# Performance work log

Hardware: AMD Instinct MI355X
Metric: run time of the kernel (lower is better)

Reference implementation:

```python
import jax, jax.numpy as jnp
import numpy as np

B, T, DIN, DM, NC = 8, 4096, 1024, 256, 157
DILS = (1, 2, 4, 8, 16)


def _conv1(w, x, b=None):
    # 1x1 conv: w [out,in], x [B,in,T] -> [B,out,T]
    y = jnp.einsum('oi,bit->bot', w, x)
    return y if b is None else y + b[None, :, None]


def _dal(x, wq, wk, wv, d):
    # Dilated 3-tap multiplicative local attention (DAL block, groups=1).
    # Taps in the zero-padded (pad=d) sequence at offsets 0, d, 2d == positions t-d, t, t+d.
    _, _, T_ = x.shape
    xp = jnp.pad(x, ((0, 0), (0, 0), (d, d)))
    q = _conv1(wq, x)                 # [B,C,T]
    kp = _conv1(wk, xp)               # [B,C,T+2d]
    vp = _conv1(wv, xp)
    k = jnp.stack([kp[:, :, 0:T_], kp[:, :, d:T_ + d], kp[:, :, 2 * d:T_ + 2 * d]], axis=-1)  # [B,C,T,3]
    v = jnp.stack([vp[:, :, 0:T_], vp[:, :, d:T_ + d], vp[:, :, 2 * d:T_ + 2 * d]], axis=-1)
    attn = jax.nn.softmax(q[..., None] * k, axis=-1)  # softmax over the 3 taps
    return jnp.sum(attn * v, axis=-1)  # [B,C,T]


def _fwd(x, mask, bottle0_w, bottle0_b,
         dal1_wq, dal1_wk, dal1_wv, bottle1_w, bottle1_b,
         dal2_wq, dal2_wk, dal2_wv, bottle2_w, bottle2_b,
         dal3_wq, dal3_wk, dal3_wv, bottle3_w, bottle3_b,
         dal4_wq, dal4_wk, dal4_wv, bottle4_w, bottle4_b,
         dal5_wq, dal5_wk, dal5_wv, bottle5_w, bottle5_b,
         bottle6_w, bottle6_b):
    m = mask[:, 0:1, :]
    out = _conv1(bottle0_w, x, bottle0_b)
    layers = [
        (dal1_wq, dal1_wk, dal1_wv, bottle1_w, bottle1_b),
        (dal2_wq, dal2_wk, dal2_wv, bottle2_w, bottle2_b),
        (dal3_wq, dal3_wk, dal3_wv, bottle3_w, bottle3_b),
        (dal4_wq, dal4_wk, dal4_wv, bottle4_w, bottle4_b),
        (dal5_wq, dal5_wk, dal5_wv, bottle5_w, bottle5_b),
    ]
    # Dropout layers are identity in eval mode.
    for (wq, wk, wv, bw, bb), d in zip(layers, DILS):
        h = jax.nn.relu(_dal(out, wq, wk, wv, d))
        h = _conv1(bw, h, bb)
        out = (out + h) * m
    return _conv1(bottle6_w, out, bottle6_b) * m  # [B,NC,T]


def setup_inputs() -> dict:
    key = jax.random.key(0)
    ks = jax.random.split(key, 32)
    s = 0.05
    inp = {}
    inp['x'] = jax.random.normal(ks[0], (B, DIN, T), jnp.float32)
    inp['mask'] = jnp.ones((B, 1, T), jnp.float32)
    inp['bottle0_w'] = jax.random.normal(ks[1], (DM, DIN), jnp.float32) * s
    inp['bottle0_b'] = jnp.zeros((DM,), jnp.float32)
    i = 2
    for l in range(1, 6):
        inp['dal%d_wq' % l] = jax.random.normal(ks[i], (DM, DM), jnp.float32) * s; i += 1
        inp['dal%d_wk' % l] = jax.random.normal(ks[i], (DM, DM), jnp.float32) * s; i += 1
        inp['dal%d_wv' % l] = jax.random.normal(ks[i], (DM, DM), jnp.float32) * s; i += 1
        inp['bottle%d_w' % l] = jax.random.normal(ks[i], (DM, DM), jnp.float32) * s; i += 1
        inp['bottle%d_b' % l] = jnp.zeros((DM,), jnp.float32)
    inp['bottle6_w'] = jax.random.normal(ks[i], (NC, DM), jnp.float32) * s
    inp['bottle6_b'] = jnp.zeros((NC,), jnp.float32)
    return inp


def reference(x, mask, bottle0_w, bottle0_b,
              dal1_wq, dal1_wk, dal1_wv, bottle1_w, bottle1_b,
              dal2_wq, dal2_wk, dal2_wv, bottle2_w, bottle2_b,
              dal3_wq, dal3_wk, dal3_wv, bottle3_w, bottle3_b,
              dal4_wq, dal4_wk, dal4_wv, bottle4_w, bottle4_b,
              dal5_wq, dal5_wk, dal5_wv, bottle5_w, bottle5_b,
              bottle6_w, bottle6_b):
    return _fwd(x, mask, bottle0_w, bottle0_b,
                dal1_wq, dal1_wk, dal1_wv, bottle1_w, bottle1_b,
                dal2_wq, dal2_wk, dal2_wv, bottle2_w, bottle2_b,
                dal3_wq, dal3_wk, dal3_wv, bottle3_w, bottle3_b,
                dal4_wq, dal4_wk, dal4_wv, bottle4_w, bottle4_b,
                dal5_wq, dal5_wk, dal5_wv, bottle5_w, bottle5_b,
                bottle6_w, bottle6_b)
```

## Files before the change

### kernel.cpp

```cpp
#include <hip/hip_runtime.h>
#include <hip/hip_bf16.h>
#include <stdint.h>

#define T_LEN 4096
#define B_SZ  8
#define D_IN  1024
#define D_M   256
#define N_C   157

typedef __attribute__((ext_vector_type(8))) short short8;
typedef __attribute__((ext_vector_type(4))) float floatx4;

static __device__ __forceinline__ unsigned short f2bf(float f) {
  unsigned u = __float_as_uint(f);
  u += 0x7FFFu + ((u >> 16) & 1u);
  return (unsigned short)(u >> 16);
}
static __device__ __forceinline__ float bf2f(unsigned short h) {
  return __uint_as_float(((unsigned)h) << 16);
}

static __device__ __forceinline__ void gl_lds16(const unsigned short* g,
                                                unsigned short* l) {
  __builtin_amdgcn_global_load_lds(
      (const __attribute__((address_space(1))) unsigned int*)g,
      (__attribute__((address_space(3))) unsigned int*)l, 16, 0, 0);
}

struct WSeg { const float* src; int n; int off; };
struct WPrepArgs { WSeg seg[22]; };

__global__ void wprep_kernel(WPrepArgs a, unsigned short* __restrict__ wbuf) {
  WSeg s = a.seg[blockIdx.x];
  for (int i = (blockIdx.y << 8) + threadIdx.x; i < s.n; i += (gridDim.y << 8))
    wbuf[s.off + i] = f2bf(s.src[i]);
}

__global__ void transpose_xT(const float* __restrict__ x,
                             unsigned short* __restrict__ xT) {
  __shared__ float tile[64][65];
  const int t0 = blockIdx.x << 6;
  const int i0 = blockIdx.y << 6;
  const int b  = blockIdx.z;
  const int tid = threadIdx.x;
  {
    const int row = tid >> 2;
    const int cc  = (tid & 3) << 4;
    const float* src = x + ((size_t)b * D_IN + (i0 + row)) * T_LEN + t0 + cc;
#pragma unroll
    for (int p = 0; p < 4; ++p) {
      float4 v = *(const float4*)(src + p * 4);
      tile[row][cc + p * 4 + 0] = v.x;
      tile[row][cc + p * 4 + 1] = v.y;
      tile[row][cc + p * 4 + 2] = v.z;
      tile[row][cc + p * 4 + 3] = v.w;
    }
  }
  __syncthreads();
#pragma unroll
  for (int it = 0; it < 2; ++it) {
    const int task = tid + (it << 8);
    const int tr = task >> 3;
    const int ic = (task & 7) << 3;
    short8 o;
#pragma unroll
    for (int j = 0; j < 8; ++j) o[j] = (short)f2bf(tile[ic + j][tr]);
    *(short8*)(xT + ((size_t)b * T_LEN + (t0 + tr)) * D_IN + i0 + ic) = o;
  }
}

template<bool ATTN, bool HAS_BIAS, bool HAS_RES, bool HAS_MASK,
         bool WRITE_BF16, bool OUT_CT_F32>
__global__ __launch_bounds__(256)
void gemm_kernel(const unsigned short* __restrict__ Xact,
                 const unsigned short* __restrict__ W,
                 const float* __restrict__ bias,
                 const unsigned short* __restrict__ residB,
                 const float* __restrict__ mask,
                 float* __restrict__ outF,
                 unsigned short* __restrict__ outB,
                 int K, int Mw, int dil) {
  __shared__ unsigned short sA[128 * 64];
  __shared__ unsigned short sB[128 * 64];

  const int n0 = blockIdx.x << 7;
  const int t0 = blockIdx.y << 7;
  const int b  = blockIdx.z;
  const int tid = threadIdx.x;
  const int wv   = tid >> 6;
  const int lane = tid & 63;
  const int wm = (wv >> 1) << 6;
  const int wn = (wv & 1) << 6;
  const int fm = lane & 15;
  const int fq = lane >> 4;
  const int lrow = lane >> 3;
  const int cbg8 = (((lane & 7) ^ lrow) << 3);

  const unsigned short* Xb =
      Xact + (size_t)b * T_LEN * (size_t)(ATTN ? 768 : K);

  const short8 z8 = {0, 0, 0, 0, 0, 0, 0, 0};
  const floatx4 fz = {0.f, 0.f, 0.f, 0.f};
  floatx4 acc[4][4];
#pragma unroll
  for (int i = 0; i < 4; ++i)
#pragma unroll
    for (int j = 0; j < 4; ++j) acc[i][j] = fz;

  for (int kk = 0; kk < K; kk += 64) {
    if constexpr (ATTN) {
#pragma unroll
      for (int it = 0; it < 4; ++it) {
        int c = tid + (it << 8);
        int m = c >> 3;
        int cb = c & 7;
        int ch = kk + (cb << 3);
        int t = t0 + m;
        const unsigned short* base = Xb + (size_t)t * 768 + ch;
        short8 qv = *(const short8*)(base);
        short8 kc = *(const short8*)(base + 256);
        short8 vc = *(const short8*)(base + 512);
        short8 km = z8, kp = z8, vm = z8, vp = z8;
        const long off = (long)dil * 768;
        if (t >= dil) {
          km = *(const short8*)(base - off + 256);
          vm = *(const short8*)(base - off + 512);
        }
        if (t + dil < T_LEN) {
          kp = *(const short8*)(base + off + 256);
          vp = *(const short8*)(base + off + 512);
        }
        short8 o;
#pragma unroll
        for (int e = 0; e < 8; ++e) {
          float q  = bf2f((unsigned short)qv[e]);
          float s0 = q * bf2f((unsigned short)km[e]);
          float s1 = q * bf2f((unsigned short)kc[e]);
          float s2 = q * bf2f((unsigned short)kp[e]);
          float mx = fmaxf(s0, fmaxf(s1, s2));
          float e0 = __expf(s0 - mx), e1 = __expf(s1 - mx), e2 = __expf(s2 - mx);
          float num = e0 * bf2f((unsigned short)vm[e]) +
                      e1 * bf2f((unsigned short)vc[e]) +
                      e2 * bf2f((unsigned short)vp[e]);
          float r = num / (e0 + e1 + e2);
          o[e] = (short)f2bf(fmaxf(r, 0.0f));
        }
        *(short8*)&sA[(m << 6) + ((cb ^ (m & 7)) << 3)] = o;
      }
    } else {
#pragma unroll
      for (int p = 0; p < 4; ++p) {
        const int slot = (p << 2) + wv;
        gl_lds16(Xb + (size_t)(t0 + (slot << 3) + lrow) * K + kk + cbg8,
                 sA + slot * 512);
      }
    }
#pragma unroll
    for (int p = 0; p < 4; ++p) {
      const int slot = (p << 2) + wv;
      gl_lds16(W + (size_t)(n0 + (slot << 3) + lrow) * K + kk + cbg8,
               sB + slot * 512);
    }
    __syncthreads();
#pragma unroll
    for (int ks = 0; ks < 64; ks += 32) {
      const int cbase = ((fq + (ks >> 3)) ^ (fm & 7)) << 3;
      short8 af[4], bfr[4];
#pragma unroll
      for (int i = 0; i < 4; ++i)
        af[i] = *(short8*)&sA[((wm + (i << 4) + fm) << 6) + cbase];
#pragma unroll
      for (int j = 0; j < 4; ++j)
        bfr[j] = *(short8*)&sB[((wn + (j << 4) + fm) << 6) + cbase];
#pragma unroll
      for (int i = 0; i < 4; ++i)
#pragma unroll
        for (int j = 0; j < 4; ++j)
          acc[i][j] = __builtin_amdgcn_mfma_f32_16x16x32_bf16(
              af[i], bfr[j], acc[i][j], 0, 0, 0);
    }
    __syncthreads();
  }

#pragma unroll
  for (int i = 0; i < 4; ++i) {
#pragma unroll
    for (int j = 0; j < 4; ++j) {
      const int co = n0 + wn + (j << 4) + fm;
      if (co >= Mw) continue;
      const float bi = HAS_BIAS ? bias[co] : 0.0f;
#pragma unroll
      for (int r = 0; r < 4; ++r) {
        const int t = t0 + wm + (i << 4) + (fq << 2) + r;
        float val = acc[i][j][r] + bi;
        const size_t idx = ((size_t)b * T_LEN + t) * (size_t)Mw + co;
        if (HAS_RES) val += bf2f(residB[idx]);
        if (HAS_MASK) val *= mask[(size_t)b * T_LEN + t];
        if (OUT_CT_F32)
          outF[(size_t)b * Mw * T_LEN + (size_t)co * T_LEN + t] = val;
        if (WRITE_BF16) outB[idx] = f2bf(val);
      }
    }
  }
}

extern "C" void kernel_launch(void* const* d_in, const int* in_sizes, int n_in,
                              void* d_out, int out_size, void* d_ws, size_t ws_size,
                              hipStream_t stream) {
  const float* x    = (const float*)d_in[0];
  const float* mask = (const float*)d_in[1];

  char* ws = (char*)d_ws;
  unsigned short* xT   = (unsigned short*)ws;
  unsigned short* qkv  = xT;
  unsigned short* outB = (unsigned short*)(ws + 67108864);
  unsigned short* wbuf = (unsigned short*)(ws + 83886080);

  const int WB0  = 0;
  const int WQKV = 262144;
  const int WBT  = 1245184;
  const int WB6  = 1572864;

  WPrepArgs pa;
  int si = 0;
  pa.seg[si++] = { (const float*)d_in[2], 262144, WB0 };
  for (int l = 0; l < 5; ++l) {
    int bi = 4 + l * 5;
    pa.seg[si++] = { (const float*)d_in[bi + 0], 65536, WQKV + l * 196608 };
    pa.seg[si++] = { (const float*)d_in[bi + 1], 65536, WQKV + l * 196608 + 65536 };
    pa.seg[si++] = { (const float*)d_in[bi + 2], 65536, WQKV + l * 196608 + 131072 };
    pa.seg[si++] = { (const float*)d_in[bi + 3], 65536, WBT + l * 65536 };
  }
  pa.seg[si++] = { (const float*)d_in[29], 40192, WB6 };

  wprep_kernel<<<dim3(22, 64), 256, 0, stream>>>(pa, wbuf);
  transpose_xT<<<dim3(64, 16, 8), 256, 0, stream>>>(x, xT);

  gemm_kernel<false, true, false, false, true, false>
      <<<dim3(2, 32, 8), 256, 0, stream>>>(
          xT, wbuf + WB0, (const float*)d_in[3], nullptr, mask,
          nullptr, outB, 1024, 256, 0);

  const int dils[5] = {1, 2, 4, 8, 16};
  for (int l = 0; l < 5; ++l) {
    int bi = 4 + l * 5;
    gemm_kernel<false, false, false, false, true, false>
        <<<dim3(6, 32, 8), 256, 0, stream>>>(
            outB, wbuf + WQKV + l * 196608, nullptr, nullptr, mask,
            nullptr, qkv, 256, 768, 0);
    gemm_kernel<true, true, true, true, true, false>
        <<<dim3(2, 32, 8), 256, 0, stream>>>(
            qkv, wbuf + WBT + l * 65536, (const float*)d_in[bi + 4], outB, mask,
            nullptr, outB, 256, 256, dils[l]);
  }

  gemm_kernel<false, true, false, true, false, true>
      <<<dim3(2, 32, 8), 256, 0, stream>>>(
          outB, wbuf + WB6, (const float*)d_in[30], nullptr, mask,
          (float*)d_out, nullptr, 256, 157, 0);
}
```

Measured before the change: 674.6 us.

## Double-buffer GEMM LDS tiles, shrink tile to 64x128, swap operands for final output

Adds double buffering to the GEMM main loop: the next K-slice is staged into a second LDS buffer while the current one feeds MFMA, which removes one barrier per iteration. The block tile shrinks from 128x128 to 64 time steps by 128 channels, so the grid doubles and occupancy rises, at the cost of more weight reloads. The final classifier GEMM now swaps operands so the weight rows become the M dimension and time is contiguous, giving coalesced stores to the [B,NC,T] float output. In exchange, register and LDS use per block change and the attention path recomputes its softmax on smaller tiles.

```diff
diff --git a/kernel.cpp b/kernel.cpp
--- a/kernel.cpp
+++ b/kernel.cpp
@@ -70,7 +70,7 @@
 }
 
 template<bool ATTN, bool HAS_BIAS, bool HAS_RES, bool HAS_MASK,
-         bool WRITE_BF16, bool OUT_CT_F32>
+         bool WRITE_BF16, bool SWAP_CT>
 __global__ __launch_bounds__(256)
 void gemm_kernel(const unsigned short* __restrict__ Xact,
                  const unsigned short* __restrict__ W,
@@ -80,38 +80,41 @@
                  float* __restrict__ outF,
                  unsigned short* __restrict__ outB,
                  int K, int Mw, int dil) {
-  __shared__ unsigned short sA[128 * 64];
-  __shared__ unsigned short sB[128 * 64];
-
-  const int n0 = blockIdx.x << 7;
-  const int t0 = blockIdx.y << 7;
+  __shared__ unsigned short sA[2][64 * 64];
+  __shared__ unsigned short sB[2][128 * 64];
+
+  const int bx = blockIdx.x;
+  const int t0 = blockIdx.y << (SWAP_CT ? 7 : 6);
   const int b  = blockIdx.z;
-  const int tid = threadIdx.x;
+  const int tid  = threadIdx.x;
   const int wv   = tid >> 6;
   const int lane = tid & 63;
-  const int wm = (wv >> 1) << 6;
-  const int wn = (wv & 1) << 6;
-  const int fm = lane & 15;
-  const int fq = lane >> 4;
+  const int wn   = wv << 5;
+  const int fm   = lane & 15;
+  const int fq   = lane >> 4;
   const int lrow = lane >> 3;
   const int cbg8 = (((lane & 7) ^ lrow) << 3);
 
   const unsigned short* Xb =
       Xact + (size_t)b * T_LEN * (size_t)(ATTN ? 768 : K);
+  const unsigned short* srcA =
+      SWAP_CT ? (W + (size_t)(bx << 6) * K) : (Xb + (size_t)t0 * K);
+  const unsigned short* srcB =
+      SWAP_CT ? (Xb + (size_t)t0 * K) : (W + (size_t)(bx << 7) * K);
 
   const short8 z8 = {0, 0, 0, 0, 0, 0, 0, 0};
   const floatx4 fz = {0.f, 0.f, 0.f, 0.f};
-  floatx4 acc[4][4];
+  floatx4 acc[4][2];
 #pragma unroll
   for (int i = 0; i < 4; ++i)
 #pragma unroll
-    for (int j = 0; j < 4; ++j) acc[i][j] = fz;
-
-  for (int kk = 0; kk < K; kk += 64) {
+    for (int j = 0; j < 2; ++j) acc[i][j] = fz;
+
+  auto stage = [&](int kk, int bufi) {
     if constexpr (ATTN) {
 #pragma unroll
-      for (int it = 0; it < 4; ++it) {
-        int c = tid + (it << 8);
+      for (int itp = 0; itp < 2; ++itp) {
+        int c = tid + (itp << 8);
         int m = c >> 3;
         int cb = c & 7;
         int ch = kk + (cb << 3);
@@ -145,60 +148,83 @@
           float r = num / (e0 + e1 + e2);
           o[e] = (short)f2bf(fmaxf(r, 0.0f));
         }
-        *(short8*)&sA[(m << 6) + ((cb ^ (m & 7)) << 3)] = o;
+        *(short8*)&sA[bufi][(m << 6) + ((cb ^ (m & 7)) << 3)] = o;
       }
     } else {
 #pragma unroll
-      for (int p = 0; p < 4; ++p) {
+      for (int p = 0; p < 2; ++p) {
         const int slot = (p << 2) + wv;
-        gl_lds16(Xb + (size_t)(t0 + (slot << 3) + lrow) * K + kk + cbg8,
-                 sA + slot * 512);
+        gl_lds16(srcA + (size_t)((slot << 3) + lrow) * K + kk + cbg8,
+                 &sA[bufi][slot * 512]);
       }
     }
 #pragma unroll
     for (int p = 0; p < 4; ++p) {
       const int slot = (p << 2) + wv;
-      gl_lds16(W + (size_t)(n0 + (slot << 3) + lrow) * K + kk + cbg8,
-               sB + slot * 512);
-    }
+      gl_lds16(srcB + (size_t)((slot << 3) + lrow) * K + kk + cbg8,
+               &sB[bufi][slot * 512]);
+    }
+  };
+
+  const int niter = K >> 6;
+  stage(0, 0);
+  for (int it = 0; it < niter; ++it) {
+    const int p = it & 1;
     __syncthreads();
+    if (it + 1 < niter) stage((it + 1) << 6, 1 - p);
 #pragma unroll
     for (int ks = 0; ks < 64; ks += 32) {
       const int cbase = ((fq + (ks >> 3)) ^ (fm & 7)) << 3;
-      short8 af[4], bfr[4];
+      short8 af[4], bfr[2];
 #pragma unroll
       for (int i = 0; i < 4; ++i)
-        af[i] = *(short8*)&sA[((wm + (i << 4) + fm) << 6) + cbase];
-#pragma unroll
-      for (int j = 0; j < 4; ++j)
-        bfr[j] = *(short8*)&sB[((wn + (j << 4) + fm) << 6) + cbase];
+        af[i] = *(short8*)&sA[p][(((i << 4) + fm) << 6) + cbase];
+#pragma unroll
+      for (int j = 0; j < 2; ++j)
+        bfr[j] = *(short8*)&sB[p][((wn + (j << 4) + fm) << 6) + cbase];
 #pragma unroll
       for (int i = 0; i < 4; ++i)
 #pragma unroll
-        for (int j = 0; j < 4; ++j)
+        for (int j = 0; j < 2; ++j)
           acc[i][j] = __builtin_amdgcn_mfma_f32_16x16x32_bf16(
               af[i], bfr[j], acc[i][j], 0, 0, 0);
     }
-    __syncthreads();
-  }
-
-#pragma unroll
-  for (int i = 0; i < 4; ++i) {
-#pragma unroll
-    for (int j = 0; j < 4; ++j) {
-      const int co = n0 + wn + (j << 4) + fm;
-      if (co >= Mw) continue;
-      const float bi = HAS_BIAS ? bias[co] : 0.0f;
+  }
+
+  if constexpr (SWAP_CT) {
+#pragma unroll
+    for (int i = 0; i < 4; ++i) {
 #pragma unroll
       for (int r = 0; r < 4; ++r) {
-        const int t = t0 + wm + (i << 4) + (fq << 2) + r;
-        float val = acc[i][j][r] + bi;
-        const size_t idx = ((size_t)b * T_LEN + t) * (size_t)Mw + co;
-        if (HAS_RES) val += bf2f(residB[idx]);
-        if (HAS_MASK) val *= mask[(size_t)b * T_LEN + t];
-        if (OUT_CT_F32)
-          outF[(size_t)b * Mw * T_LEN + (size_t)co * T_LEN + t] = val;
-        if (WRITE_BF16) outB[idx] = f2bf(val);
+        const int o = (bx << 6) + (i << 4) + (fq << 2) + r;
+        if (o >= Mw) continue;
+        const float bi = HAS_BIAS ? bias[o] : 0.0f;
+#pragma unroll
+        for (int j = 0; j < 2; ++j) {
+          const int t = t0 + wn + (j << 4) + fm;
+          float val = acc[i][j][r] + bi;
+          if (HAS_MASK) val *= mask[(size_t)b * T_LEN + t];
+          outF[((size_t)b * Mw + o) * T_LEN + t] = val;
+        }
+      }
+    }
+  } else {
+#pragma unroll
+    for (int i = 0; i < 4; ++i) {
+#pragma unroll
+      for (int j = 0; j < 2; ++j) {
+        const int co = (bx << 7) + wn + (j << 4) + fm;
+        if (co >= Mw) continue;
+        const float bi = HAS_BIAS ? bias[co] : 0.0f;
+#pragma unroll
+        for (int r = 0; r < 4; ++r) {
+          const int t = t0 + (i << 4) + (fq << 2) + r;
+          float val = acc[i][j][r] + bi;
+          const size_t idx = ((size_t)b * T_LEN + t) * (size_t)Mw + co;
+          if (HAS_RES) val += bf2f(residB[idx]);
+          if (HAS_MASK) val *= mask[(size_t)b * T_LEN + t];
+          if (WRITE_BF16) outB[idx] = f2bf(val);
+        }
       }
     }
   }
@@ -237,7 +263,7 @@
   transpose_xT<<<dim3(64, 16, 8), 256, 0, stream>>>(x, xT);
 
   gemm_kernel<false, true, false, false, true, false>
-      <<<dim3(2, 32, 8), 256, 0, stream>>>(
+      <<<dim3(2, 64, 8), 256, 0, stream>>>(
           xT, wbuf + WB0, (const float*)d_in[3], nullptr, mask,
           nullptr, outB, 1024, 256, 0);
 
@@ -245,17 +271,17 @@
   for (int l = 0; l < 5; ++l) {
     int bi = 4 + l * 5;
     gemm_kernel<false, false, false, false, true, false>
-        <<<dim3(6, 32, 8), 256, 0, stream>>>(
+        <<<dim3(6, 64, 8), 256, 0, stream>>>(
             outB, wbuf + WQKV + l * 196608, nullptr, nullptr, mask,
             nullptr, qkv, 256, 768, 0);
     gemm_kernel<true, true, true, true, true, false>
-        <<<dim3(2, 32, 8), 256, 0, stream>>>(
+        <<<dim3(2, 64, 8), 256, 0, stream>>>(
             qkv, wbuf + WBT + l * 65536, (const float*)d_in[bi + 4], outB, mask,
             nullptr, outB, 256, 256, dils[l]);
   }
 
   gemm_kernel<false, true, false, true, false, true>
-      <<<dim3(2, 32, 8), 256, 0, stream>>>(
+      <<<dim3(3, 32, 8), 256, 0, stream>>>(
           outB, wbuf + WB6, (const float*)d_in[30], nullptr, mask,
           (float*)d_out, nullptr, 256, 157, 0);
 }
```

Result: faster. 653.5 us (-3.1%).
